# Performance work log

Measured on AMD Instinct MI355X. Metric: run time of the kernel, lower is better.

## Reference

```python
import jax, jax.numpy as jnp
import numpy as np

K = 3       # kernel_size
STRIDE = 1


def setup_inputs() -> dict:
    key = jax.random.key(0)
    k1, k2, k3 = jax.random.split(key, 3)
    B, C, H, W = 128, 64, 32, 32
    O = 64
    OH = (H - K) // STRIDE + 1  # 30
    OW = (W - K) // STRIDE + 1  # 30
    x = jax.random.normal(k1, (B, C, H, W), dtype=jnp.float32)
    weight = jax.random.normal(k2, (O, C, OH, OW, K, K), dtype=jnp.float32)
    bias = jax.random.normal(k3, (O, OH, OW), dtype=jnp.float32)
    return {"x": x, "weight": weight, "bias": bias}


def reference(x, weight, bias):
    # x: [B, C, H, W]; weight: [O, C, OH, OW, K, K]; bias: [O, OH, OW]
    O, C, OH, OW, _, _ = weight.shape
    # Extract all k x k patches in one pass: [B, C*K*K, OH, OW],
    # feature axis ordered (C, kh, kw) with spatial fastest.
    patches = jax.lax.conv_general_dilated_patches(
        x, filter_shape=(K, K), window_strides=(STRIDE, STRIDE), padding="VALID"
    )
    # Faithful to torch einsum 'bcih,coih->bo': the region's channel axis is
    # contracted against the weight's FIRST axis (nominal out_channels), and the
    # output channel is the weight's SECOND axis (requires C == O).
    # Rearrange weight -> [C*K*K (contract), O (output), OH, OW].
    w = jnp.transpose(weight, (0, 4, 5, 1, 2, 3)).reshape(C * K * K, O, OH, OW)
    out = jnp.einsum("bpij,poij->boij", patches, w) + bias[None]
    return out  # [B, O, OH, OW]
```

## Files before the change

### kernel.cpp

```cpp
#include <hip/hip_runtime.h>


typedef __bf16 bf16x8 __attribute__((ext_vector_type(8)));
typedef float f32x4 __attribute__((ext_vector_type(4)));
typedef unsigned long long u64;
typedef unsigned int u32t;
typedef unsigned short u16t;

struct __attribute__((packed, aligned(8))) uf4 { f32x4 v; };
struct __attribute__((packed, aligned(4))) uf4a { f32x4 v; };
struct __attribute__((packed, aligned(8))) uf2 { float2 v; };
struct __attribute__((packed, aligned(4))) uq2 { u64 x, y; };
struct __attribute__((aligned(16))) ull2 { u64 x, y; };

__device__ __forceinline__ u16t f2bf(float f) {
  union { float f; u32t u; } v; v.f = f;
  u32t r = v.u + 0x7fffu + ((v.u >> 16) & 1u);
  return (u16t)(r >> 16);
}
__device__ __forceinline__ u32t pk2(float a, float b) {
  return (u32t)f2bf(a) | ((u32t)f2bf(b) << 16);
}
__device__ __forceinline__ bf16x8 mk_af(u64 lo, u64 hi) {
  union { u64 q[2]; bf16x8 v; } u;
  u.q[0] = lo; u.q[1] = hi;
  return u.v;
}


__global__ __launch_bounds__(256) void lcl_prep_x3(const float* __restrict__ x,
                                                   u16t* __restrict__ Xb) {
  int gid = blockIdx.x * 256 + threadIdx.x;
  int b  = gid & 127;
  int ch = gid >> 7;
  const float* src = x + (size_t)b * 65536 + ch * 32;
  u64 qv[8];
#pragma unroll
  for (int s = 0; s < 8; ++s) {
    f32x4 a = ((const uf4*)(src + s * 4))->v;
    qv[s] = (u64)pk2(a[0], a[1]) | ((u64)pk2(a[2], a[3]) << 32);
  }
  u16t* dst = Xb + ((size_t)ch * 5 * 128 + b) * 8;
  ull2 w;
  w.x = qv[0];                          w.y = qv[1];                          *(ull2*)(dst)        = w;
  w.x = (qv[1] >> 32) | (qv[2] << 32);  w.y = (qv[2] >> 32) | (qv[3] << 32);  *(ull2*)(dst + 1024) = w;
  w.x = qv[3];                          w.y = qv[4];                          *(ull2*)(dst + 2048) = w;
  w.x = (qv[4] >> 32) | (qv[5] << 32);  w.y = (qv[5] >> 32) | (qv[6] << 32);  *(ull2*)(dst + 3072) = w;
  w.x = qv[6];                          w.y = qv[7];                          *(ull2*)(dst + 4096) = w;
}

__global__ __launch_bounds__(256, 2) void lcl_main10(
    const u16t* __restrict__ Xb, const float* __restrict__ wgt,
    const float* __restrict__ bias, float* __restrict__ out) {
  int bid = blockIdx.x;
  int xcd = bid & 7, sg = bid >> 3;
  int t = xcd * 75 + sg;
  int jg = t % 5;
  int r  = t / 5;
  int bg = r & 1, og = (r >> 1) & 1, i = r >> 2;
  int j0 = jg * 6;
  int ij0 = i * 30 + j0;

  __shared__ __align__(16) u16t Bt[2 * 20480];

  const int tid  = threadIdx.x;
  const int wave = tid >> 6;
  const int lane = tid & 63;
  const int lrow = lane & 15;
  const int q    = lane >> 4;

  {
    u64* zp = (u64*)Bt;
#pragma unroll
    for (int k = 0; k < 40; ++k) zp[tid + k * 256] = 0ull;
  }

  const int b_x = bg * 64 + wave * 16 + lrow;
  const char* xbase = (const char*)Xb;
  u32t xoff[3][2];
#pragma unroll
  for (int s = 0; s < 3; ++s)
#pragma unroll
    for (int tt = 0; tt < 2; ++tt) {
      int g = s * 8 + q * 2 + tt, cc = g / 3, kh = g - cc * 3;
      xoff[s][tt] = (u32t)((((cc * 32 + (i + kh)) * 5 + jg) * 128 + b_x) * 16);
    }

  const int e8 = tid & 7, g8 = tid >> 3;
  const int o_w = og * 32 + g8;
  const int FO0 = e8 * 4;
  const int FO1 = 22 + e8 * 4;
  int Pofs[8];
#pragma unroll
  for (int jm = 0; jm < 8; ++jm) {
    int F = ((jm & 4) ? FO1 : FO0) + (jm & 3);
    Pofs[jm] = (F / 9) * 3344 + ((F % 9) / 3) * 4 + (F % 3);
  }
  const float* wb = wgt + (size_t)o_w * 8100 + ij0 * 9;

  ull2  rq[3][2];
  f32x4 wreg[16];

#define LOAD_CHUNK10(C0)                                                    \
  {                                                                         \
    const size_t xadv = (size_t)(C0) * 327680;                              \
    _Pragma("unroll") for (int s = 0; s < 3; ++s)                           \
    _Pragma("unroll") for (int tt = 0; tt < 2; ++tt)                        \
      rq[s][tt] = *(const ull2*)(xbase + xadv + xoff[s][tt]);               \
    _Pragma("unroll") for (int k = 0; k < 16; ++k) {                        \
      const int p_ = k >> 1;                                                \
      const float* wq = wb + (size_t)((C0) + p_) * 518400 +                 \
                        ((k & 1) ? FO1 : FO0);                              \
      wreg[k] = ((const uf4a*)wq)->v;                                       \
    }                                                                       \
  }

  f32x4 acc[6][2];
#pragma unroll
  for (int a = 0; a < 6; ++a)
#pragma unroll
    for (int n = 0; n < 2; ++n) acc[a][n] = f32x4{0.f, 0.f, 0.f, 0.f};

  LOAD_CHUNK10(0)
  __syncthreads();

  for (int chunk = 0; chunk < 8; ++chunk) {
    u16t* Bb = Bt + (chunk & 1) * 20480 + g8 * 104;
#pragma unroll
    for (int k = 0; k < 16; ++k) {
      const int p_ = k >> 1, h_ = k & 1;
#pragma unroll
      for (int m = 0; m < 4; ++m)
        (Bb + Pofs[h_ * 4 + m])[p_ * 12] = f2bf(wreg[k][m]);
    }

    u64 rb[3][2][2];
#pragma unroll
    for (int s = 0; s < 3; ++s)
#pragma unroll
      for (int tt = 0; tt < 2; ++tt) {
        rb[s][tt][0] = rq[s][tt].x;
        rb[s][tt][1] = rq[s][tt].y;
      }

    __syncthreads();

    if (chunk < 7) LOAD_CHUNK10((chunk + 1) * 8)

#pragma unroll
    for (int s = 0; s < 3; ++s) {
#pragma unroll
      for (int jj = 0; jj < 6; ++jj) {
        bf16x8 bfr0 = *(const bf16x8*)&Bt[(chunk & 1) * 20480 + jj * 3344 +
                                          lrow * 104 + s * 32 + q * 8];
        bf16x8 bfr1 = *(const bf16x8*)&Bt[(chunk & 1) * 20480 + jj * 3344 +
                                          (16 + lrow) * 104 + s * 32 + q * 8];
        u64 lo, hi;
        if (jj == 0) {
          lo = rb[s][0][0];
          hi = rb[s][1][0];
        } else if (jj < 4) {
          lo = (rb[s][0][0] >> (16 * jj)) | (rb[s][0][1] << (64 - 16 * jj));
          hi = (rb[s][1][0] >> (16 * jj)) | (rb[s][1][1] << (64 - 16 * jj));
        } else if (jj == 4) {
          lo = rb[s][0][1];
          hi = rb[s][1][1];
        } else {
          lo = rb[s][0][1] >> 16;
          hi = rb[s][1][1] >> 16;
        }
        bf16x8 af = mk_af(lo, hi);
        acc[jj][0] = __builtin_amdgcn_mfma_f32_16x16x32_bf16(af, bfr0, acc[jj][0], 0, 0, 0);
        acc[jj][1] = __builtin_amdgcn_mfma_f32_16x16x32_bf16(af, bfr1, acc[jj][1], 0, 0, 0);
      }
    }
  }

  const int b0 = bg * 64 + wave * 16 + q * 4;
#pragma unroll
  for (int nt = 0; nt < 2; ++nt) {
    int o = og * 32 + nt * 16 + lrow;
    const float* bp = bias + o * 900 + ij0;
    f32x4 b03 = ((const uf4*)bp)->v;
    float2 b45 = ((const uf2*)(bp + 4))->v;
#pragma unroll
    for (int rr = 0; rr < 4; ++rr) {
      float* op = out + (size_t)(b0 + rr) * 57600 + o * 900 + ij0;
      f32x4 r03;
      r03[0] = acc[0][nt][rr] + b03[0];
      r03[1] = acc[1][nt][rr] + b03[1];
      r03[2] = acc[2][nt][rr] + b03[2];
      r03[3] = acc[3][nt][rr] + b03[3];
      float2 r45;
      r45.x = acc[4][nt][rr] + b45.x;
      r45.y = acc[5][nt][rr] + b45.y;
      ((uf4*)op)->v = r03;
      ((uf2*)(op + 4))->v = r45;
    }
  }
}

__global__ __launch_bounds__(256) void lcl_prep_x(const float* __restrict__ x,
                                                  u16t* __restrict__ Xb) {
  int gid = blockIdx.x * 256 + threadIdx.x;
  int b  = gid & 127;
  int ch = gid >> 7;
  const float* src = x + (size_t)b * 65536 + ch * 32;
  u16t* dst = Xb + (size_t)gid * 32;
  u64 qv[8];
#pragma unroll
  for (int s = 0; s < 8; ++s) {
    f32x4 a = ((const uf4*)(src + s * 4))->v;
    qv[s] = (u64)pk2(a[0], a[1]) | ((u64)pk2(a[2], a[3]) << 32);
  }
#pragma unroll
  for (int s = 0; s < 4; ++s) {
    ull2 w; w.x = qv[2 * s]; w.y = qv[2 * s + 1];
    *(ull2*)(dst + s * 8) = w;
  }
}

__global__ __launch_bounds__(256, 2) void lcl_main9(
    const u16t* __restrict__ Xb, const float* __restrict__ wgt,
    const float* __restrict__ bias, float* __restrict__ out) {
  int bid = blockIdx.x;
  int xcd = bid & 7, sg = bid >> 3;
  int t = xcd * 75 + sg;
  int jg = t % 5;
  int r  = t / 5;
  int bg = r & 1, og = (r >> 1) & 1, i = r >> 2;
  int j0 = jg * 6;
  int ij0 = i * 30 + j0;

  __shared__ __align__(16) u16t Bt[2 * 6 * 32 * 104];

  const int tid  = threadIdx.x;
  const int wave = tid >> 6;
  const int lane = tid & 63;
  const int lrow = lane & 15;
  const int q    = lane >> 4;

  {
    u64* zp = (u64*)Bt;
#pragma unroll
    for (int k = 0; k < 39; ++k) zp[tid + k * 256] = 0ull;
  }

  const int b_x = bg * 64 + wave * 16 + lrow;
  const char* xbase = (const char*)Xb;
  u32t xoff[3][2];
#pragma unroll
  for (int s = 0; s < 3; ++s)
#pragma unroll
    for (int tt = 0; tt < 2; ++tt) {
      int g = s * 8 + q * 2 + tt, cc = g / 3, kh = g - cc * 3;
      xoff[s][tt] = (u32t)(((cc * 32 + (i + kh)) * 128 + b_x) * 64 + j0 * 2);
    }

  const int e8 = tid & 7, g8 = tid >> 3;
  const int o_w = og * 32 + g8;
  const int FO0 = e8 * 4;
  const int FO1 = 22 + e8 * 4;
  int Pofs[8];
#pragma unroll
  for (int jm = 0; jm < 8; ++jm) {
    int F = ((jm & 4) ? FO1 : FO0) + (jm & 3);
    Pofs[jm] = (F / 9) * 3328 + ((F % 9) / 3) * 4 + (F % 3);
  }
  const float* wb = wgt + (size_t)o_w * 8100 + ij0 * 9;

  uq2   rq[3][2];
  f32x4 wreg[16];

#define LOAD_CHUNK9(C0)                                                     \
  {                                                                         \
    const size_t xadv = (size_t)(C0) * 262144;                              \
    _Pragma("unroll") for (int s = 0; s < 3; ++s)                           \
    _Pragma("unroll") for (int tt = 0; tt < 2; ++tt)                        \
      rq[s][tt] = *(const uq2*)(xbase + xadv + xoff[s][tt]);                \
    _Pragma("unroll") for (int k = 0; k < 16; ++k) {                        \
      const int p_ = k >> 1;                                                \
      const float* wq = wb + (size_t)((C0) + p_) * 518400 +                 \
                        ((k & 1) ? FO1 : FO0);                              \
      wreg[k] = ((const uf4a*)wq)->v;                                       \
    }                                                                       \
  }

  f32x4 acc[6][2];
#pragma unroll
  for (int a = 0; a < 6; ++a)
#pragma unroll
    for (int n = 0; n < 2; ++n) acc[a][n] = f32x4{0.f, 0.f, 0.f, 0.f};

  LOAD_CHUNK9(0)
  __syncthreads();

  for (int chunk = 0; chunk < 8; ++chunk) {
    u16t* Bb = Bt + (chunk & 1) * 19968 + g8 * 104;
#pragma unroll
    for (int k = 0; k < 16; ++k) {
      const int p_ = k >> 1, h_ = k & 1;
#pragma unroll
      for (int m = 0; m < 4; ++m)
        (Bb + Pofs[h_ * 4 + m])[p_ * 12] = f2bf(wreg[k][m]);
    }

    u64 rb[3][2][2];
#pragma unroll
    for (int s = 0; s < 3; ++s)
#pragma unroll
      for (int tt = 0; tt < 2; ++tt) {
        rb[s][tt][0] = rq[s][tt].x;
        rb[s][tt][1] = rq[s][tt].y;
      }

    __syncthreads();

    if (chunk < 7) LOAD_CHUNK9((chunk + 1) * 8)

#pragma unroll
    for (int s = 0; s < 3; ++s) {
#pragma unroll
      for (int jj = 0; jj < 6; ++jj) {
        bf16x8 bfr0 = *(const bf16x8*)&Bt[(chunk & 1) * 19968 + jj * 3328 +
                                          lrow * 104 + s * 32 + q * 8];
        bf16x8 bfr1 = *(const bf16x8*)&Bt[(chunk & 1) * 19968 + jj * 3328 +
                                          (16 + lrow) * 104 + s * 32 + q * 8];
        u64 lo, hi;
        if (jj == 0) {
          lo = rb[s][0][0];
          hi = rb[s][1][0];
        } else if (jj < 4) {
          lo = (rb[s][0][0] >> (16 * jj)) | (rb[s][0][1] << (64 - 16 * jj));
          hi = (rb[s][1][0] >> (16 * jj)) | (rb[s][1][1] << (64 - 16 * jj));
        } else if (jj == 4) {
          lo = rb[s][0][1];
          hi = rb[s][1][1];
        } else {
          lo = rb[s][0][1] >> 16;
          hi = rb[s][1][1] >> 16;
        }
        bf16x8 af = mk_af(lo, hi);
        acc[jj][0] = __builtin_amdgcn_mfma_f32_16x16x32_bf16(af, bfr0, acc[jj][0], 0, 0, 0);
        acc[jj][1] = __builtin_amdgcn_mfma_f32_16x16x32_bf16(af, bfr1, acc[jj][1], 0, 0, 0);
      }
    }
  }

  const int b0 = bg * 64 + wave * 16 + q * 4;
#pragma unroll
  for (int nt = 0; nt < 2; ++nt) {
    int o = og * 32 + nt * 16 + lrow;
    const float* bp = bias + o * 900 + ij0;
    f32x4 b03 = ((const uf4*)bp)->v;
    float2 b45 = ((const uf2*)(bp + 4))->v;
#pragma unroll
    for (int rr = 0; rr < 4; ++rr) {
      float* op = out + (size_t)(b0 + rr) * 57600 + o * 900 + ij0;
      f32x4 r03;
      r03[0] = acc[0][nt][rr] + b03[0];
      r03[1] = acc[1][nt][rr] + b03[1];
      r03[2] = acc[2][nt][rr] + b03[2];
      r03[3] = acc[3][nt][rr] + b03[3];
      float2 r45;
      r45.x = acc[4][nt][rr] + b45.x;
      r45.y = acc[5][nt][rr] + b45.y;
      ((uf4*)op)->v = r03;
      ((uf2*)(op + 4))->v = r45;
    }
  }
}

__global__ __launch_bounds__(256, 2) void lcl_r4(
    const float* __restrict__ x, const float* __restrict__ wgt,
    const float* __restrict__ bias, float* __restrict__ out) {
  int blk = blockIdx.x;
  int xcd = blk & 7, sg = blk >> 3;
  int t = xcd * 56 + (xcd < 2 ? xcd : 2) + sg;
  int i = t / 15;
  int j0 = (t % 15) * 2;
  int ij0 = i * 30 + j0;

  __shared__ __align__(16) u16t Bt[2 * 2 * 64 * 104];

  const int tid  = threadIdx.x;
  const int wave = tid >> 6;
  const int lane = tid & 63;
  const int lrow = lane & 15;
  const int q    = lane >> 4;

  {
    u64* zp = (u64*)Bt;
#pragma unroll
    for (int k = 0; k < 26; ++k) zp[tid + k * 256] = 0ull;
  }

  int xoffF[3][2];
#pragma unroll
  for (int s = 0; s < 3; ++s)
#pragma unroll
    for (int tt = 0; tt < 2; ++tt) {
      int g = s * 8 + q * 2 + tt, cc = g / 3, kh = g - cc * 3;
      xoffF[s][tt] = cc * 1024 + kh * 32;
    }
  const float* xb0 = x + (wave * 32 + lrow) * 65536 + i * 32 + j0;
  const float* xb1 = xb0 + 16 * 65536;

  const int o_w = tid & 63;
  const float* wb0 = wgt + (size_t)wave * 518400 + o_w * 8100 + ij0 * 9;
  const float* wb1 = wb0 + (size_t)4 * 518400;

  f32x4 av[2][3][2];
  f32x4 wv[2][5];

#define LOAD_CHUNK4(C0)                                                       \
  {                                                                           \
    const float* xc0 = xb0 + (C0) * 1024;                                     \
    const float* xc1 = xb1 + (C0) * 1024;                                     \
    _Pragma("unroll") for (int s = 0; s < 3; ++s)                             \
    _Pragma("unroll") for (int tt = 0; tt < 2; ++tt) {                        \
      av[0][s][tt] = ((const uf4*)(xc0 + xoffF[s][tt]))->v;                   \
      av[1][s][tt] = ((const uf4*)(xc1 + xoffF[s][tt]))->v;                   \
    }                                                                         \
    const float* w0 = wb0 + (size_t)(C0) * 518400;                            \
    const float* w1 = wb1 + (size_t)(C0) * 518400;                            \
    _Pragma("unroll") for (int e = 0; e < 4; ++e) {                           \
      wv[0][e] = ((const uf4*)(w0 + e * 4))->v;                               \
      wv[1][e] = ((const uf4*)(w1 + e * 4))->v;                               \
    }                                                                         \
    wv[0][4] = ((const uf4*)(w0 + 14))->v;                                    \
    wv[1][4] = ((const uf4*)(w1 + 14))->v;                                    \
  }

  f32x4 acc[2][2][4];
#pragma unroll
  for (int a = 0; a < 2; ++a)
#pragma unroll
    for (int b = 0; b < 2; ++b)
#pragma unroll
      for (int c = 0; c < 4; ++c) acc[a][b][c] = f32x4{0.f, 0.f, 0.f, 0.f};

  LOAD_CHUNK4(0)

  for (int chunk = 0; chunk < 8; ++chunk) {
    u16t* B = Bt + (chunk & 1) * 13312;
#pragma unroll
    for (int p = 0; p < 2; ++p) {
      int ccl = wave + 4 * p;
      u16t* Bp = B + o_w * 104 + ccl * 12;
      *(u32t*)&Bp[0] = pk2(wv[p][0][0], wv[p][0][1]);
      Bp[2]  = f2bf(wv[p][0][2]);
      Bp[4]  = f2bf(wv[p][0][3]);
      Bp[5]  = f2bf(wv[p][1][0]);
      Bp[6]  = f2bf(wv[p][1][1]);
      *(u32t*)&Bp[8] = pk2(wv[p][1][2], wv[p][1][3]);
      Bp[10] = f2bf(wv[p][2][0]);
      u16t* Bq = Bp + 6656;
      *(u32t*)&Bq[0] = pk2(wv[p][2][1], wv[p][2][2]);
      Bq[2]  = f2bf(wv[p][2][3]);
      Bq[4]  = f2bf(wv[p][3][0]);
      Bq[5]  = f2bf(wv[p][3][1]);
      Bq[6]  = f2bf(wv[p][3][2]);
      *(u32t*)&Bq[8] = pk2(wv[p][3][3], wv[p][4][2]);
      Bq[10] = f2bf(wv[p][4][3]);
    }

    u64 rb[2][3][2];
#pragma unroll
    for (int mt = 0; mt < 2; ++mt)
#pragma unroll
      for (int s = 0; s < 3; ++s)
#pragma unroll
        for (int tt = 0; tt < 2; ++tt) {
          const f32x4 vv = av[mt][s][tt];
          rb[mt][s][tt] = (u64)pk2(vv[0], vv[1]) | ((u64)pk2(vv[2], vv[3]) << 32);
        }

    __syncthreads();

    if (chunk < 7) LOAD_CHUNK4((chunk + 1) * 8)

#pragma unroll
    for (int s = 0; s < 3; ++s) {
      bf16x8 bfr[2][4];
#pragma unroll
      for (int jj = 0; jj < 2; ++jj)
#pragma unroll
        for (int nt = 0; nt < 4; ++nt)
          bfr[jj][nt] = *reinterpret_cast<const bf16x8*>(
              &B[jj * 6656 + (nt * 16 + lrow) * 104 + s * 32 + q * 8]);
#pragma unroll
      for (int mt = 0; mt < 2; ++mt)
#pragma unroll
        for (int jj = 0; jj < 2; ++jj) {
          u64 lo = rb[mt][s][0] >> (jj * 16);
          u64 hi = rb[mt][s][1] >> (jj * 16);
          bf16x8 af = mk_af(lo, hi);
#pragma unroll
          for (int nt = 0; nt < 4; ++nt)
            acc[mt][jj][nt] = __builtin_amdgcn_mfma_f32_16x16x32_bf16(
                af, bfr[jj][nt], acc[mt][jj][nt], 0, 0, 0);
        }
    }
  }

#pragma unroll
  for (int nt = 0; nt < 4; ++nt) {
    int o = nt * 16 + lrow;
    float2 bv = *(const float2*)(bias + o * 900 + ij0);
#pragma unroll
    for (int mt = 0; mt < 2; ++mt) {
#pragma unroll
      for (int rr = 0; rr < 4; ++rr) {
        int b = wave * 32 + mt * 16 + q * 4 + rr;
        float2 res;
        res.x = acc[mt][0][nt][rr] + bv.x;
        res.y = acc[mt][1][nt][rr] + bv.y;
        *(float2*)(out + b * 57600 + o * 900 + ij0) = res;
      }
    }
  }
}

extern "C" void kernel_launch(void* const* d_in, const int* in_sizes, int n_in,
                              void* d_out, int out_size, void* d_ws,
                              size_t ws_size, hipStream_t stream) {
  const float* x    = (const float*)d_in[0];
  const float* wgt  = (const float*)d_in[1];
  const float* bias = (const float*)d_in[2];
  float* out        = (float*)d_out;
  if (ws_size >= (size_t)20971520 && d_ws != nullptr) {
    lcl_prep_x3<<<dim3(1024), dim3(256), 0, stream>>>(x, (u16t*)d_ws);
    lcl_main10<<<dim3(600), dim3(256), 0, stream>>>((const u16t*)d_ws, wgt, bias, out);
  } else if (ws_size >= (size_t)16777216 && d_ws != nullptr) {
    lcl_prep_x<<<dim3(1024), dim3(256), 0, stream>>>(x, (u16t*)d_ws);
    lcl_main9<<<dim3(600), dim3(256), 0, stream>>>((const u16t*)d_ws, wgt, bias, out);
  } else {
    lcl_r4<<<dim3(450), dim3(256), 0, stream>>>(x, wgt, bias, out);
  }
}
```

Before: 276.6 us.

## Merge batch halves into 512-thread blocks sharing one weight tile

Each block now has 512 threads (8 waves) and covers all 128 batch rows for its (i, j-group, o-group) tile, where before two blocks each handled 64 batch rows. The converted bf16 weight tile in LDS is therefore shared by twice as many waves, which halves the redundant global weight loads and conversions. The weight tile is also re-laid-out in LDS so each MFMA B-fragment is read as a contiguous lane*8 slice, and weight loading uses 14 of every 16 threads with 16-byte loads. The XCD block-mapping is adjusted for the 300-block grid. This trades fewer, larger blocks against occupancy and load balance.

```diff
diff --git a/kernel.cpp b/kernel.cpp
--- a/kernel.cpp
+++ b/kernel.cpp
@@ -49,19 +49,19 @@
   w.x = qv[6];                          w.y = qv[7];                          *(ull2*)(dst + 4096) = w;
 }
 
-__global__ __launch_bounds__(256, 2) void lcl_main10(
+__global__ __launch_bounds__(512, 4) void lcl_main11(
     const u16t* __restrict__ Xb, const float* __restrict__ wgt,
     const float* __restrict__ bias, float* __restrict__ out) {
   int bid = blockIdx.x;
   int xcd = bid & 7, sg = bid >> 3;
-  int t = xcd * 75 + sg;
+  int t = (xcd < 4 ? xcd * 38 : 152 + (xcd - 4) * 37) + sg;
   int jg = t % 5;
   int r  = t / 5;
-  int bg = r & 1, og = (r >> 1) & 1, i = r >> 2;
+  int og = r & 1, i = r >> 1;
   int j0 = jg * 6;
   int ij0 = i * 30 + j0;
 
-  __shared__ __align__(16) u16t Bt[2 * 20480];
+  __shared__ __align__(16) u16t Bt[2 * 18432];
 
   const int tid  = threadIdx.x;
   const int wave = tid >> 6;
@@ -72,10 +72,10 @@
   {
     u64* zp = (u64*)Bt;
 #pragma unroll
-    for (int k = 0; k < 40; ++k) zp[tid + k * 256] = 0ull;
-  }
-
-  const int b_x = bg * 64 + wave * 16 + lrow;
+    for (int k = 0; k < 18; ++k) zp[tid + k * 512] = 0ull;
+  }
+
+  const int b_x = wave * 16 + lrow;
   const char* xbase = (const char*)Xb;
   u32t xoff[3][2];
 #pragma unroll
@@ -86,32 +86,35 @@
       xoff[s][tt] = (u32t)((((cc * 32 + (i + kh)) * 5 + jg) * 128 + b_x) * 16);
     }
 
-  const int e8 = tid & 7, g8 = tid >> 3;
-  const int o_w = og * 32 + g8;
-  const int FO0 = e8 * 4;
-  const int FO1 = 22 + e8 * 4;
-  int Pofs[8];
-#pragma unroll
-  for (int jm = 0; jm < 8; ++jm) {
-    int F = ((jm & 4) ? FO1 : FO0) + (jm & 3);
-    Pofs[jm] = (F / 9) * 3344 + ((F % 9) / 3) * 4 + (F % 3);
-  }
-  const float* wb = wgt + (size_t)o_w * 8100 + ij0 * 9;
+  const int e16 = tid & 15, g16 = tid >> 4 & 31;
+  const bool wact = e16 < 14;
+  const int e16b = (e16 * 16 > 200) ? 200 : e16 * 16;
+  const int F0 = e16b >> 2;
+  const int nt_o = g16 >> 4, lr_o = g16 & 15;
+  int kk4_m[4], Bm_m[4];
+#pragma unroll
+  for (int m = 0; m < 4; ++m) {
+    int F = F0 + m;
+    int dj = F / 9, rem = F - dj * 9;
+    int kh = rem / 3, kw = rem - kh * 3;
+    kk4_m[m] = kh * 4 + kw;
+    Bm_m[m] = (dj * 6 + nt_o * 3) * 512 + lr_o * 8;
+  }
+  const char* wb = (const char*)(wgt + (size_t)(og * 32 + g16) * 8100 +
+                                 ij0 * 9) + e16b;
 
   ull2  rq[3][2];
-  f32x4 wreg[16];
-
-#define LOAD_CHUNK10(C0)                                                    \
+  f32x4 wv8[8];
+
+#define LOAD_CHUNK11(C0)                                                    \
   {                                                                         \
     const size_t xadv = (size_t)(C0) * 327680;                              \
     _Pragma("unroll") for (int s = 0; s < 3; ++s)                           \
     _Pragma("unroll") for (int tt = 0; tt < 2; ++tt)                        \
       rq[s][tt] = *(const ull2*)(xbase + xadv + xoff[s][tt]);               \
-    _Pragma("unroll") for (int k = 0; k < 16; ++k) {                        \
-      const int p_ = k >> 1;                                                \
-      const float* wq = wb + (size_t)((C0) + p_) * 518400 +                 \
-                        ((k & 1) ? FO1 : FO0);                              \
-      wreg[k] = ((const uf4a*)wq)->v;                                       \
+    if (wact) {                                                             \
+      _Pragma("unroll") for (int p = 0; p < 8; ++p)                         \
+        wv8[p] = ((const uf4a*)(wb + (size_t)((C0) + p) * 2073600))->v;     \
     }                                                                       \
   }
 
@@ -121,17 +124,20 @@
 #pragma unroll
     for (int n = 0; n < 2; ++n) acc[a][n] = f32x4{0.f, 0.f, 0.f, 0.f};
 
-  LOAD_CHUNK10(0)
+  LOAD_CHUNK11(0)
   __syncthreads();
 
   for (int chunk = 0; chunk < 8; ++chunk) {
-    u16t* Bb = Bt + (chunk & 1) * 20480 + g8 * 104;
-#pragma unroll
-    for (int k = 0; k < 16; ++k) {
-      const int p_ = k >> 1, h_ = k & 1;
-#pragma unroll
-      for (int m = 0; m < 4; ++m)
-        (Bb + Pofs[h_ * 4 + m])[p_ * 12] = f2bf(wreg[k][m]);
+    u16t* Bb = Bt + (chunk & 1) * 18432;
+
+    if (wact) {
+#pragma unroll
+      for (int p = 0; p < 8; ++p)
+#pragma unroll
+        for (int m = 0; m < 4; ++m) {
+          int kp = p * 12 + kk4_m[m];
+          Bb[Bm_m[m] + ((kp >> 3) << 7) + (kp & 7)] = f2bf(wv8[p][m]);
+        }
     }
 
     u64 rb[3][2][2];
@@ -145,16 +151,14 @@
 
     __syncthreads();
 
-    if (chunk < 7) LOAD_CHUNK10((chunk + 1) * 8)
+    if (chunk < 7) LOAD_CHUNK11((chunk + 1) * 8)
 
 #pragma unroll
     for (int s = 0; s < 3; ++s) {
 #pragma unroll
       for (int jj = 0; jj < 6; ++jj) {
-        bf16x8 bfr0 = *(const bf16x8*)&Bt[(chunk & 1) * 20480 + jj * 3344 +
-                                          lrow * 104 + s * 32 + q * 8];
-        bf16x8 bfr1 = *(const bf16x8*)&Bt[(chunk & 1) * 20480 + jj * 3344 +
-                                          (16 + lrow) * 104 + s * 32 + q * 8];
+        bf16x8 bfr0 = *(const bf16x8*)&Bb[((jj * 6 + 0 * 3 + s) << 9) + lane * 8];
+        bf16x8 bfr1 = *(const bf16x8*)&Bb[((jj * 6 + 1 * 3 + s) << 9) + lane * 8];
         u64 lo, hi;
         if (jj == 0) {
           lo = rb[s][0][0];
@@ -176,7 +180,7 @@
     }
   }
 
-  const int b0 = bg * 64 + wave * 16 + q * 4;
+  const int b0 = wave * 16 + q * 4;
 #pragma unroll
   for (int nt = 0; nt < 2; ++nt) {
     int o = og * 32 + nt * 16 + lrow;
@@ -531,7 +535,7 @@
   float* out        = (float*)d_out;
   if (ws_size >= (size_t)20971520 && d_ws != nullptr) {
     lcl_prep_x3<<<dim3(1024), dim3(256), 0, stream>>>(x, (u16t*)d_ws);
-    lcl_main10<<<dim3(600), dim3(256), 0, stream>>>((const u16t*)d_ws, wgt, bias, out);
+    lcl_main11<<<dim3(300), dim3(512), 0, stream>>>((const u16t*)d_ws, wgt, bias, out);
   } else if (ws_size >= (size_t)16777216 && d_ws != nullptr) {
     lcl_prep_x<<<dim3(1024), dim3(256), 0, stream>>>(x, (u16t*)d_ws);
     lcl_main9<<<dim3(600), dim3(256), 0, stream>>>((const u16t*)d_ws, wgt, bias, out);
```

Result: slower. 398.8 us (+44.2%).
